# Optimization experiments

Measured on AMD Instinct MI355X. Metric: run time of the kernel, lower is better.

## Reference

```python
import jax, jax.numpy as jnp
import numpy as np

B, T, V, DIN = 16, 360, 25, 2
H, NCLS, NAUX = 128, 12, 8
NSPLITS = NAUX + 1
N = T * V        # nodes per graph
E = 72000        # edges per graph
EPS = 1e-5       # BatchNorm eps


def _norm_coefs(edge_index, n):
    # GCNConv default: add self-loops, symmetric normalization D^-1/2 (A+I) D^-1/2
    src, dst = edge_index[0], edge_index[1]
    loops = jnp.arange(n, dtype=src.dtype)
    src = jnp.concatenate([src, loops])
    dst = jnp.concatenate([dst, loops])
    deg = jnp.zeros((n,), jnp.float32).at[dst].add(1.0)
    dinv = jax.lax.rsqrt(deg)
    return src, dst, dinv[src] * dinv[dst]


def _gcn_bn_relu(x, W, b, gamma, beta, src, dst, coef):
    # x: [B, N, din] -> [B, N, dout]; GCNConv then BatchNorm1d (batch stats) + ReLU
    h = x @ W
    msg = h[:, src, :] * coef[None, :, None]          # gather + scale
    agg = jnp.zeros(h.shape, h.dtype).at[:, dst, :].add(msg) + b  # scatter-add
    mean = agg.mean(axis=(0, 1))
    var = agg.var(axis=(0, 1))                        # biased var, as torch BN fwd
    hn = (agg - mean) * jax.lax.rsqrt(var + EPS)
    return jax.nn.relu(gamma * hn + beta)


def _head(x, Wg, bg, gamma, beta, Wf, bf, src, dst, coef):
    h = _gcn_bn_relu(x, Wg, bg, gamma, beta, src, dst, coef)
    pooled = h.mean(axis=1)                           # GlobalMeanPool (equal-size graphs)
    # Dropout is identity in eval mode
    return jax.nn.log_softmax(pooled @ Wf + bf, axis=1)


def setup_inputs() -> dict:
    key = jax.random.key(0)
    ks = jax.random.split(key, 8)
    s = 0.1
    return {
        "x": jax.random.normal(ks[0], (B, T, V, DIN), jnp.float32),
        "edge_index": jax.random.randint(ks[1], (2, E), 0, N, jnp.int64 if jax.config.jax_enable_x64 else jnp.int32),
        "W_in": jax.random.normal(ks[2], (DIN, H), jnp.float32) * s,
        "b_in": jnp.zeros((H,), jnp.float32),
        "g_in": jnp.ones((H,), jnp.float32),
        "be_in": jnp.zeros((H,), jnp.float32),
        "shared_W": jax.random.normal(ks[3], (2, H, H), jnp.float32) * s,
        "shared_b": jnp.zeros((2, H), jnp.float32),
        "shared_g": jnp.ones((2, H), jnp.float32),
        "shared_be": jnp.zeros((2, H), jnp.float32),
        "main_Wg": jax.random.normal(ks[4], (H, H), jnp.float32) * s,
        "main_bg": jnp.zeros((H,), jnp.float32),
        "main_g": jnp.ones((H,), jnp.float32),
        "main_be": jnp.zeros((H,), jnp.float32),
        "main_Wf": jax.random.normal(ks[5], (H, NCLS), jnp.float32) * s,
        "main_bf": jnp.zeros((NCLS,), jnp.float32),
        "aux_Wg": jax.random.normal(ks[6], (NAUX, H, H), jnp.float32) * s,
        "aux_bg": jnp.zeros((NAUX, H), jnp.float32),
        "aux_g": jnp.ones((NAUX, H), jnp.float32),
        "aux_be": jnp.zeros((NAUX, H), jnp.float32),
        "aux_Wf": jax.random.normal(ks[7], (NAUX, H, NCLS), jnp.float32) * s,
        "aux_bf": jnp.zeros((NAUX, NCLS), jnp.float32),
    }


def reference(x, edge_index, W_in, b_in, g_in, be_in, shared_W, shared_b, shared_g,
              shared_be, main_Wg, main_bg, main_g, main_be, main_Wf, main_bf,
              aux_Wg, aux_bg, aux_g, aux_be, aux_Wf, aux_bf):
    src, dst, coef = _norm_coefs(edge_index, N)
    h = x.reshape(B, N, DIN)
    h = _gcn_bn_relu(h, W_in, b_in, g_in, be_in, src, dst, coef)
    for i in range(shared_W.shape[0]):
        h = _gcn_bn_relu(h, shared_W[i], shared_b[i], shared_g[i], shared_be[i], src, dst, coef)
    o_main = _head(h, main_Wg, main_bg, main_g, main_be, main_Wf, main_bf, src, dst, coef)
    h4 = h.reshape(B, T, V, H)
    ws = T // NSPLITS
    t = jnp.arange(T)
    outs = []
    for i in range(NSPLITS - 1):
        idx = (t + ws * (i + 1)) % T          # cyclic time shift (fi[si:si+T])
        hr = h4[:, idx].reshape(B, N, H)
        outs.append(_head(hr, aux_Wg[i], aux_bg[i], aux_g[i], aux_be[i],
                          aux_Wf[i], aux_bf[i], src, dst, coef))
    o_aux = jnp.stack(outs, axis=1)           # [B, NAUX, NCLS]
    return o_main, o_aux
```

## Files before the change

kernel.cpp:

```cpp
#include <hip/hip_runtime.h>
#include <hip/hip_bf16.h>
#include <math.h>

#define BB 16
#define TT 360
#define VV 25
#define NN 9000
#define EE 72000
#define HH 128
#define RR (NN * BB)
#define CROWS 18000
#define NTILES (RR / 64)
#define NPART0 563
#define NCLSS 12
#define EPSB 1e-5f


typedef _Float16 h4v __attribute__((ext_vector_type(4)));
typedef _Float16 h8v __attribute__((ext_vector_type(8)));
typedef float float16v __attribute__((ext_vector_type(16)));

__device__ __forceinline__ h8v cf8(unsigned packed) {
    uint4 cc = {packed, packed, packed, packed};
    return __builtin_bit_cast(h8v, cc);
}


__global__ void k_count(const int* __restrict__ ei, int* __restrict__ counts) {
    int e = blockIdx.x * 256 + threadIdx.x;
    if (e < EE) atomicAdd(&counts[ei[EE + e]], 1);
}

__global__ void k_dinv(const int* __restrict__ counts, float* __restrict__ dinv,
                       unsigned* __restrict__ d2p) {
    int n = blockIdx.x * 256 + threadIdx.x;
    if (n >= NN) return;
    float di = rsqrtf((float)(counts[n] + 1));
    dinv[n] = di;
    _Float16 d2 = (_Float16)(di * di);
    unsigned short u = __builtin_bit_cast(unsigned short, d2);
    d2p[n] = (unsigned)u | ((unsigned)u << 16);
}

__global__ void k_scan(const int* __restrict__ counts, int* __restrict__ rowptr4) {
    __shared__ int part[1024];
    int t = threadIdx.x;
    int base = t * 9;
    int loc[9];
    int s = 0;
#pragma unroll
    for (int i = 0; i < 9; i++) {
        int idx = base + i;
        int v = (idx < NN) ? ((counts[idx] + 3) & ~3) : 0;
        loc[i] = s;
        s += v;
    }
    part[t] = s;
    __syncthreads();
    for (int d = 1; d < 1024; d <<= 1) {
        int v = (t >= d) ? part[t - d] : 0;
        __syncthreads();
        part[t] += v;
        __syncthreads();
    }
    int excl = (t == 0) ? 0 : part[t - 1];
#pragma unroll
    for (int i = 0; i < 9; i++) {
        int idx = base + i;
        if (idx < NN) rowptr4[idx] = excl + loc[i];
    }
    if (t == 1023) rowptr4[NN] = part[1023];
}

__global__ void k_fill(const int* __restrict__ ei, const int* __restrict__ rowptr4,
                       int* __restrict__ cursor, const float* __restrict__ dinv,
                       int2* __restrict__ csr) {
    int e = blockIdx.x * 256 + threadIdx.x;
    if (e >= EE) return;
    int s = ei[e], d = ei[EE + e];
    int slot = rowptr4[d] + atomicAdd(&cursor[d], 1);
    _Float16 cfh = (_Float16)(dinv[s] * dinv[d]);
    unsigned short u = __builtin_bit_cast(unsigned short, cfh);
    int2 e2;
    e2.x = s;
    e2.y = (int)((unsigned)u | ((unsigned)u << 16));
    csr[slot] = e2;
}

__global__ void k_pad(const int* __restrict__ rowptr4, const int* __restrict__ cursor,
                      int2* __restrict__ csr) {
    int n = blockIdx.x * 256 + threadIdx.x;
    if (n >= NN) return;
    int beg = rowptr4[n] + cursor[n];
    int end = rowptr4[n + 1];
    int2 z;
    z.x = n;
    z.y = 0;
    for (int e = beg; e < end; e++) csr[e] = z;
}

__global__ void k_wcvt(const float* __restrict__ sW, const float* __restrict__ mW,
                       const float* __restrict__ aW, _Float16* __restrict__ Wh) {
    int idx = blockIdx.x * 256 + threadIdx.x;
    if (idx >= 11 * 16384) return;
    int l = idx >> 14, r = idx & 16383;
    int k = r >> 7, c = r & 127;
    const float* src = (l < 2) ? sW + (size_t)l * 16384
                               : ((l == 2) ? mW : aW + (size_t)(l - 3) * 16384);
    Wh[(size_t)l * 16384 + c * 128 + k] = (_Float16)src[k * 128 + c];
}

__global__ void k_prop2(const float* __restrict__ x, float* __restrict__ P0,
                        const int* __restrict__ rowptr4, const int2* __restrict__ csr,
                        const float* __restrict__ dinv) {
    int n = blockIdx.x * 256 + threadIdx.x;
    if (n >= NN) return;
    int b = blockIdx.y;
    const float* xb = x + (size_t)b * NN * 2;
    float d2 = dinv[n] * dinv[n];
    float a0 = d2 * xb[2 * n], a1 = d2 * xb[2 * n + 1];
    int beg = rowptr4[n], end = rowptr4[n + 1];
    for (int j = beg; j < end; j++) {
        int2 e2 = csr[j];
        int s = e2.x;
        unsigned short u = (unsigned short)((unsigned)e2.y & 0xffffu);
        float cf = (float)__builtin_bit_cast(_Float16, u);
        a0 += cf * xb[2 * s];
        a1 += cf * xb[2 * s + 1];
    }
    float* Pb = P0 + (size_t)(n * BB + b) * 2;
    Pb[0] = a0;
    Pb[1] = a1;
}

__global__ void __launch_bounds__(256) k_mm2(const float* __restrict__ P0,
                                             _Float16* __restrict__ A,
                                             const float* __restrict__ W,
                                             const float* __restrict__ bias,
                                             float* __restrict__ pS1, float* __restrict__ pS2) {
    __shared__ float L1[256][8], L2[256][8];
    int t = threadIdx.x;
    int cg = t & 15, c8 = cg * 8;
    float wv0[8], wv1[8], bv[8];
#pragma unroll
    for (int j = 0; j < 8; j++) {
        wv0[j] = W[c8 + j];
        wv1[j] = W[HH + c8 + j];
        bv[j] = bias[c8 + j];
    }
    float s1[8], s2[8];
#pragma unroll
    for (int j = 0; j < 8; j++) { s1[j] = 0.f; s2[j] = 0.f; }
    for (int idx = blockIdx.x * 256 + t; idx < RR * 16; idx += gridDim.x * 256) {
        int Rr = idx >> 4;
        int q = Rr / CROWS;
        int rr = Rr - q * CROWS;
        int n = rr >> 1;
        int b = q * 2 + (rr & 1);
        float p0 = P0[((size_t)n * BB + b) * 2], p1 = P0[((size_t)n * BB + b) * 2 + 1];
        h8v o;
#pragma unroll
        for (int j = 0; j < 8; j++) {
            float v = p0 * wv0[j] + p1 * wv1[j] + bv[j];
            s1[j] += v;
            s2[j] += v * v;
            o[j] = (_Float16)v;
        }
        *(h8v*)(A + (size_t)Rr * HH + c8) = o;
    }
#pragma unroll
    for (int j = 0; j < 8; j++) { L1[t][j] = s1[j]; L2[t][j] = s2[j]; }
    __syncthreads();
    if (t < 16) {
#pragma unroll
        for (int g = 1; g < 16; g++)
#pragma unroll
            for (int j = 0; j < 8; j++) {
                s1[j] = (g == 1 ? L1[t][j] : s1[j]) + L1[t + 16 * g][j];
                s2[j] = (g == 1 ? L2[t][j] : s2[j]) + L2[t + 16 * g][j];
            }
#pragma unroll
        for (int j = 0; j < 8; j++) {
            pS1[(size_t)(t * 8 + j) * NPART0 + blockIdx.x] = s1[j];
            pS2[(size_t)(t * 8 + j) * NPART0 + blockIdx.x] = s2[j];
        }
    }
}

__global__ void __launch_bounds__(256) k_act(const _Float16* __restrict__ A,
                                             _Float16* __restrict__ HP,
                                             const float* __restrict__ scale,
                                             const float* __restrict__ shiftv) {
    int i = blockIdx.x * 256 + threadIdx.x;
    int c8 = (i & 15) * 8;
    h8v v = *(const h8v*)(A + (size_t)i * 8);
    h8v o;
#pragma unroll
    for (int j = 0; j < 8; j++) {
        float f = (float)v[j] * scale[c8 + j] + shiftv[c8 + j];
        o[j] = (_Float16)fmaxf(f, 0.f);
    }
    *(h8v*)(HP + (size_t)i * 8) = o;
}

__global__ void __launch_bounds__(256) k_gather3(const _Float16* __restrict__ h,
                                                 _Float16* B0, _Float16* B1, _Float16* B2,
                                                 const int* __restrict__ rowptr4,
                                                 const int2* __restrict__ csr,
                                                 const unsigned* __restrict__ d2p, int shbase) {
    int z = blockIdx.y;
    _Float16* Pz = (z == 0) ? B0 : ((z == 1) ? B1 : B2);
    int shn = shbase + z * 1000;
    int t = threadIdx.x;
    int q = blockIdx.x & 7;
    int ng4 = blockIdx.x >> 3;
    int wv = t >> 6, l = t & 63;
    int n = ng4 * 4 + wv;
    int half = l >> 5, li = l & 31;
    const _Float16* hb = h + (size_t)q * CROWS * HH + (size_t)li * 8;
    int pn = n + shn;
    if (pn >= NN) pn -= NN;
    h8v acc;
    {
        h8v v = *(const h8v*)(hb + (size_t)pn * 2 * HH);
        acc = v * cf8(half ? 0u : d2p[n]);
    }
    int beg = rowptr4[n], end = rowptr4[n + 1];
    int e = beg;
    for (; e + 8 <= end; e += 8) {
        int4 m0 = *(const int4*)(csr + e);
        int4 m1 = *(const int4*)(csr + e + 2);
        int4 m2 = *(const int4*)(csr + e + 4);
        int4 m3 = *(const int4*)(csr + e + 6);
        int s0 = (half ? m0.z : m0.x) + shn; if (s0 >= NN) s0 -= NN;
        int s1 = (half ? m1.z : m1.x) + shn; if (s1 >= NN) s1 -= NN;
        int s2 = (half ? m2.z : m2.x) + shn; if (s2 >= NN) s2 -= NN;
        int s3 = (half ? m3.z : m3.x) + shn; if (s3 >= NN) s3 -= NN;
        h8v v0 = *(const h8v*)(hb + (size_t)s0 * 2 * HH);
        h8v v1 = *(const h8v*)(hb + (size_t)s1 * 2 * HH);
        h8v v2 = *(const h8v*)(hb + (size_t)s2 * 2 * HH);
        h8v v3 = *(const h8v*)(hb + (size_t)s3 * 2 * HH);
        acc += v0 * cf8((unsigned)(half ? m0.w : m0.y));
        acc += v1 * cf8((unsigned)(half ? m1.w : m1.y));
        acc += v2 * cf8((unsigned)(half ? m2.w : m2.y));
        acc += v3 * cf8((unsigned)(half ? m3.w : m3.y));
    }
    if (e < end) {
        int4 m0 = *(const int4*)(csr + e);
        int4 m1 = *(const int4*)(csr + e + 2);
        int s0 = (half ? m0.z : m0.x) + shn; if (s0 >= NN) s0 -= NN;
        int s1 = (half ? m1.z : m1.x) + shn; if (s1 >= NN) s1 -= NN;
        h8v v0 = *(const h8v*)(hb + (size_t)s0 * 2 * HH);
        h8v v1 = *(const h8v*)(hb + (size_t)s1 * 2 * HH);
        acc += v0 * cf8((unsigned)(half ? m0.w : m0.y));
        acc += v1 * cf8((unsigned)(half ? m1.w : m1.y));
    }
    {
        int4 ai = __builtin_bit_cast(int4, acc);
        int4 bi4;
        bi4.x = __shfl_xor(ai.x, 32, 64);
        bi4.y = __shfl_xor(ai.y, 32, 64);
        bi4.z = __shfl_xor(ai.z, 32, 64);
        bi4.w = __shfl_xor(ai.w, 32, 64);
        acc += __builtin_bit_cast(h8v, bi4);
    }
    if (half == 0) {
        *(h8v*)(Pz + ((size_t)q * CROWS + (size_t)n * 2) * HH + (size_t)li * 8) = acc;
    }
}

__global__ void __launch_bounds__(256) k_mfma3(_Float16* B0, _Float16* B1, _Float16* B2,
                                               const _Float16* __restrict__ Wh_g,
                                               const float* bias0, const float* bias1,
                                               const float* bias2,
                                               float* __restrict__ pS1,
                                               float* __restrict__ pS2) {
    __shared__ float rb1[4][128], rb2[4][128];
    int z = blockIdx.y;
    _Float16* B = (z == 0) ? B0 : ((z == 1) ? B1 : B2);
    const _Float16* Wh = Wh_g + (size_t)z * 16384;
    const float* bias = (z == 0) ? bias0 : ((z == 1) ? bias1 : bias2);
    int t = threadIdx.x;
    int w = t >> 6, l = t & 63;
    int rw = w >> 1, cw = w & 1;
    int lr = l & 31, hi = l >> 5;
    size_t rbase = (size_t)blockIdx.x * 64;
    const _Float16* Pr0 = B + (rbase + rw * 32 + lr) * HH;
    const _Float16* Wc0 = Wh + (size_t)(cw * 64 + lr) * HH;
    const _Float16* Wc1 = Wh + (size_t)(cw * 64 + 32 + lr) * HH;
    float16v acc2[2];
#pragma unroll
    for (int ct = 0; ct < 2; ct++) acc2[ct] = (float16v)(0.0f);
#pragma unroll
    for (int ks = 0; ks < 8; ks++) {
        int koff = ks * 16 + hi * 8;
        h8v a0 = *(const h8v*)(Pr0 + koff);
        h8v b0 = *(const h8v*)(Wc0 + koff);
        h8v b1 = *(const h8v*)(Wc1 + koff);
        acc2[0] = __builtin_amdgcn_mfma_f32_32x32x16_f16(a0, b0, acc2[0], 0, 0, 0);
        acc2[1] = __builtin_amdgcn_mfma_f32_32x32x16_f16(a0, b1, acc2[1], 0, 0, 0);
    }
    __syncthreads();
    float bv[2] = {bias[cw * 64 + lr], bias[cw * 64 + 32 + lr]};
    float s1a[2] = {0.f, 0.f}, s2a[2] = {0.f, 0.f};
#pragma unroll
    for (int ct = 0; ct < 2; ct++) {
        int c = cw * 64 + ct * 32 + lr;
#pragma unroll
        for (int g = 0; g < 16; g++) {
            int row = rw * 32 + (g & 3) + 8 * (g >> 2) + 4 * hi;
            float v = acc2[ct][g] + bv[ct];
            s1a[ct] += v;
            s2a[ct] += v * v;
            B[(rbase + row) * HH + c] = (_Float16)v;
        }
    }
    int slot = rw * 2 + hi;
#pragma unroll
    for (int ct = 0; ct < 2; ct++) {
        int cidx = cw * 64 + ct * 32 + lr;
        rb1[slot][cidx] = s1a[ct];
        rb2[slot][cidx] = s2a[ct];
    }
    __syncthreads();
    if (t < 128) {
        float a1 = rb1[0][t] + rb1[1][t] + rb1[2][t] + rb1[3][t];
        float a2 = rb2[0][t] + rb2[1][t] + rb2[2][t] + rb2[3][t];
        pS1[((size_t)z * HH + t) * NTILES + blockIdx.x] = a1;
        pS2[((size_t)z * HH + t) * NTILES + blockIdx.x] = a2;
    }
}

__global__ void __launch_bounds__(256) k_bnfin3(const float* __restrict__ pS1,
                                                const float* __restrict__ pS2, int npart,
                                                const float* g0, const float* g1,
                                                const float* g2, const float* be0,
                                                const float* be1, const float* be2,
                                                float* __restrict__ scale,
                                                float* __restrict__ shiftv) {
    __shared__ float R1[256], R2[256];
    int z = blockIdx.x >> 7, c = blockIdx.x & 127;
    const float* g = (z == 0) ? g0 : ((z == 1) ? g1 : g2);
    const float* be = (z == 0) ? be0 : ((z == 1) ? be1 : be2);
    int t = threadIdx.x;
    const float* p1 = pS1 + ((size_t)z * HH + c) * npart;
    const float* p2 = pS2 + ((size_t)z * HH + c) * npart;
    float s1 = 0.f, s2 = 0.f;
    for (int i = t; i < npart; i += 256) {
        s1 += p1[i];
        s2 += p2[i];
    }
    R1[t] = s1;
    R2[t] = s2;
    __syncthreads();
    for (int d = 128; d > 0; d >>= 1) {
        if (t < d) {
            R1[t] += R1[t + d];
            R2[t] += R2[t + d];
        }
        __syncthreads();
    }
    if (t == 0) {
        float inv = 1.0f / (float)RR;
        float mu = R1[0] * inv;
        float var = R2[0] * inv - mu * mu;
        float sc = g[c] * rsqrtf(var + EPSB);
        scale[z * HH + c] = sc;
        shiftv[z * HH + c] = be[c] - mu * sc;
    }
}

__global__ void __launch_bounds__(256) k_pool3(const _Float16* B0, const _Float16* B1,
                                               const _Float16* B2,
                                               const float* __restrict__ scale,
                                               const float* __restrict__ shiftv,
                                               float* __restrict__ pooled) {
    __shared__ float L[256][8];
    int z = blockIdx.z;
    const _Float16* A = (z == 0) ? B0 : ((z == 1) ? B1 : B2);
    const float* sc0 = scale + z * HH;
    const float* sh0 = shiftv + z * HH;
    float* pz = pooled + (size_t)z * BB * HH;
    int t = threadIdx.x;
    int b = blockIdx.y;
    int n0 = blockIdx.x * 250;
    int ng = t >> 4, c8 = (t & 15) * 8;
    float sc[8], sh[8];
#pragma unroll
    for (int j = 0; j < 8; j++) {
        sc[j] = sc0[c8 + j];
        sh[j] = sh0[c8 + j];
    }
    const _Float16* Ab = A + ((size_t)(b >> 1) * CROWS + (b & 1)) * HH;
    float acc[8];
#pragma unroll
    for (int j = 0; j < 8; j++) acc[j] = 0.f;
    for (int n = n0 + ng; n < n0 + 250; n += 16) {
        h8v v = *(const h8v*)(Ab + (size_t)n * 2 * HH + c8);
#pragma unroll
        for (int j = 0; j < 8; j++) {
            float f = (float)v[j] * sc[j] + sh[j];
            acc[j] += fmaxf(f, 0.f);
        }
    }
#pragma unroll
    for (int j = 0; j < 8; j++) L[t][j] = acc[j];
    __syncthreads();
    if (ng == 0) {
#pragma unroll
        for (int g = 1; g < 16; g++)
#pragma unroll
            for (int j = 0; j < 8; j++) acc[j] += L[t + 16 * g][j];
#pragma unroll
        for (int j = 0; j < 8; j++) atomicAdd(&pz[b * HH + t * 8 + j], acc[j]);
    }
}

__global__ void __launch_bounds__(192) k_head_all(const float* __restrict__ pooled,
                                                  const float* __restrict__ main_Wf,
                                                  const float* __restrict__ main_bf,
                                                  const float* __restrict__ aux_Wf,
                                                  const float* __restrict__ aux_bf,
                                                  float* __restrict__ out) {
    int hd = blockIdx.x;
    const float* Wf = hd ? aux_Wf + (size_t)(hd - 1) * HH * NCLSS : main_Wf;
    const float* bf = hd ? aux_bf + (hd - 1) * NCLSS : main_bf;
    const float* pl = pooled + (size_t)hd * BB * HH;
    __shared__ float z[BB][NCLSS];
    __shared__ float lse[BB];
    int t = threadIdx.x;
    int b = t / NCLSS, j = t % NCLSS;
    if (t < BB * NCLSS) {
        float acc = bf[j];
        const float invn = 1.0f / NN;
        for (int c = 0; c < HH; c++) acc += pl[b * HH + c] * invn * Wf[c * NCLSS + j];
        z[b][j] = acc;
    }
    __syncthreads();
    if (t < BB) {
        float m = -1e30f;
        for (int j2 = 0; j2 < NCLSS; j2++) m = fmaxf(m, z[t][j2]);
        float s = 0.f;
        for (int j2 = 0; j2 < NCLSS; j2++) s += expf(z[t][j2] - m);
        lse[t] = m + logf(s);
    }
    __syncthreads();
    if (t < BB * NCLSS) {
        float* o = hd ? out + BB * NCLSS + ((size_t)b * 8 + (hd - 1)) * NCLSS + j
                      : out + b * NCLSS + j;
        *o = z[b][j] - lse[b];
    }
}


extern "C" void kernel_launch(void* const* d_in, const int* in_sizes, int n_in, void* d_out,
                              int out_size, void* d_ws, size_t ws_size, hipStream_t stream) {
    const float* x = (const float*)d_in[0];
    const int* ei = (const int*)d_in[1];
    const float* W_in = (const float*)d_in[2];
    const float* b_in = (const float*)d_in[3];
    const float* g_in = (const float*)d_in[4];
    const float* be_in = (const float*)d_in[5];
    const float* shared_W = (const float*)d_in[6];
    const float* shared_b = (const float*)d_in[7];
    const float* shared_g = (const float*)d_in[8];
    const float* shared_be = (const float*)d_in[9];
    const float* main_Wg = (const float*)d_in[10];
    const float* main_bg = (const float*)d_in[11];
    const float* main_g = (const float*)d_in[12];
    const float* main_be = (const float*)d_in[13];
    const float* main_Wf = (const float*)d_in[14];
    const float* main_bf = (const float*)d_in[15];
    const float* aux_Wg = (const float*)d_in[16];
    const float* aux_bg = (const float*)d_in[17];
    const float* aux_g = (const float*)d_in[18];
    const float* aux_be = (const float*)d_in[19];
    const float* aux_Wf = (const float*)d_in[20];
    const float* aux_bf = (const float*)d_in[21];
    float* out = (float*)d_out;

    char* w = (char*)d_ws;
    const size_t BIG = (size_t)RR * HH * 2;
    _Float16* U = (_Float16*)w;  w += BIG;
    _Float16* V = (_Float16*)w;  w += BIG;
    _Float16* P = (_Float16*)w;  w += BIG;
    _Float16* HP = (_Float16*)w; w += BIG;
    float* P0 = (float*)w;       w += (size_t)RR * 2 * 4;
    _Float16* Wh = (_Float16*)w; w += (size_t)11 * 16384 * 2;
    int2* csr = (int2*)w;        w += (size_t)102400 * 8;
    int* counts = (int*)w;       w += NN * 4;
    int* cursor = (int*)w;       w += NN * 4;
    float* dinv = (float*)w;     w += NN * 4;
    unsigned* d2p = (unsigned*)w; w += NN * 4;
    int* rowptr4 = (int*)w;      w += 36016;
    float* pS1 = (float*)w;      w += (size_t)3 * HH * NTILES * 4;
    float* pS2 = (float*)w;      w += (size_t)3 * HH * NTILES * 4;
    float* pooled = (float*)w;   w += 9 * BB * HH * 4;
    float* tscale = (float*)w;   w += 512;
    float* tshift = (float*)w;   w += 512;
    float* hscale = (float*)w;   w += 2048;
    float* hshift = (float*)w;   w += 2048;

    hipMemsetAsync(counts, 0, 2 * NN * 4, stream);
    hipMemsetAsync(pooled, 0, 9 * BB * HH * 4, stream);

    k_count<<<(EE + 255) / 256, 256, 0, stream>>>(ei, counts);
    k_dinv<<<(NN + 255) / 256, 256, 0, stream>>>(counts, dinv, d2p);
    k_scan<<<1, 1024, 0, stream>>>(counts, rowptr4);
    k_fill<<<(EE + 255) / 256, 256, 0, stream>>>(ei, rowptr4, cursor, dinv, csr);
    k_pad<<<(NN + 255) / 256, 256, 0, stream>>>(rowptr4, cursor, csr);
    k_wcvt<<<(11 * 16384 + 255) / 256, 256, 0, stream>>>(shared_W, main_Wg, aux_Wg, Wh);

    {
        dim3 g((NN + 255) / 256, BB);
        k_prop2<<<g, 256, 0, stream>>>(x, P0, rowptr4, csr, dinv);
        k_mm2<<<NPART0, 256, 0, stream>>>(P0, U, W_in, b_in, pS1, pS2);
        k_bnfin3<<<HH, 256, 0, stream>>>(pS1, pS2, NPART0, g_in, g_in, g_in, be_in, be_in,
                                         be_in, tscale, tshift);
    }

    k_act<<<RR * 16 / 256, 256, 0, stream>>>(U, HP, tscale, tshift);
    k_gather3<<<dim3(8 * 2250, 1), 256, 0, stream>>>(HP, V, V, V, rowptr4, csr, d2p, 0);
    k_mfma3<<<dim3(NTILES, 1), 256, 0, stream>>>(V, V, V, Wh, shared_b, shared_b, shared_b,
                                                 pS1, pS2);
    k_bnfin3<<<HH, 256, 0, stream>>>(pS1, pS2, NTILES, shared_g, shared_g, shared_g, shared_be,
                                     shared_be, shared_be, tscale, tshift);
    k_act<<<RR * 16 / 256, 256, 0, stream>>>(V, HP, tscale, tshift);
    k_gather3<<<dim3(8 * 2250, 1), 256, 0, stream>>>(HP, U, U, U, rowptr4, csr, d2p, 0);
    k_mfma3<<<dim3(NTILES, 1), 256, 0, stream>>>(U, U, U, Wh + 16384, shared_b + HH,
                                                 shared_b + HH, shared_b + HH, pS1, pS2);
    k_bnfin3<<<HH, 256, 0, stream>>>(pS1, pS2, NTILES, shared_g + HH, shared_g + HH,
                                     shared_g + HH, shared_be + HH, shared_be + HH,
                                     shared_be + HH, tscale, tshift);
    k_act<<<RR * 16 / 256, 256, 0, stream>>>(U, HP, tscale, tshift);

    for (int g = 0; g < 3; g++) {
        int h0 = g * 3;
        const float* bg[3];
        const float* gg[3];
        const float* be[3];
        for (int z = 0; z < 3; z++) {
            int hd = h0 + z;
            bg[z] = (hd == 0) ? main_bg : aux_bg + (hd - 1) * HH;
            gg[z] = (hd == 0) ? main_g : aux_g + (hd - 1) * HH;
            be[z] = (hd == 0) ? main_be : aux_be + (hd - 1) * HH;
        }
        k_gather3<<<dim3(8 * 2250, 3), 256, 0, stream>>>(HP, P, U, V, rowptr4, csr, d2p,
                                                         h0 * 1000);
        k_mfma3<<<dim3(NTILES, 3), 256, 0, stream>>>(P, U, V, Wh + (size_t)(2 + h0) * 16384,
                                                     bg[0], bg[1], bg[2], pS1, pS2);
        k_bnfin3<<<3 * HH, 256, 0, stream>>>(pS1, pS2, NTILES, gg[0], gg[1], gg[2], be[0],
                                             be[1], be[2], hscale, hshift);
        k_pool3<<<dim3(36, BB, 3), 256, 0, stream>>>(P, U, V, hscale, hshift,
                                                     pooled + (size_t)h0 * BB * HH);
    }
    k_head_all<<<9, 192, 0, stream>>>(pooled, main_Wf, main_bf, aux_Wf, aux_bf, out);
}
```

Measured before the change: 868.2 us.

## Recompute GEMM instead of storing pre-BN output; fuse BN-ReLU and pooling into GEMM

The GEMM kernel no longer writes its fp16 output. It only emits per-tile BatchNorm partial sums. After the statistics are finalized, a second pass recomputes the GEMM and applies bias, BN and ReLU directly, writing HP for the shared layers or accumulating the pooled means for the heads. This removes the separate activation and pooling kernels along with the round-trip store and reload of the intermediate, at the cost of doing each GEMM twice. Tiles are now laid out per graph-pair of 18000 rows, with masking on the partial last tile so the pooling parity maps to batch index.

```diff
diff --git a/kernel.cpp b/kernel.cpp
--- a/kernel.cpp
+++ b/kernel.cpp
@@ -10,13 +10,13 @@
 #define HH 128
 #define RR (NN * BB)
 #define CROWS 18000
-#define NTILES (RR / 64)
+#define TPC2 282
+#define NT3 (8 * TPC2)
 #define NPART0 563
 #define NCLSS 12
 #define EPSB 1e-5f
 
 
-typedef _Float16 h4v __attribute__((ext_vector_type(4)));
 typedef _Float16 h8v __attribute__((ext_vector_type(8)));
 typedef float float16v __attribute__((ext_vector_type(16)));
 
@@ -269,22 +269,27 @@
     }
 }
 
-__global__ void __launch_bounds__(256) k_mfma3(_Float16* B0, _Float16* B1, _Float16* B2,
-                                               const _Float16* __restrict__ Wh_g,
-                                               const float* bias0, const float* bias1,
-                                               const float* bias2,
-                                               float* __restrict__ pS1,
-                                               float* __restrict__ pS2) {
+
+__global__ void __launch_bounds__(256) k_mfmaS3(const _Float16* B0, const _Float16* B1,
+                                                const _Float16* B2,
+                                                const _Float16* __restrict__ Wh_g,
+                                                const float* bias0, const float* bias1,
+                                                const float* bias2,
+                                                float* __restrict__ pS1,
+                                                float* __restrict__ pS2) {
     __shared__ float rb1[4][128], rb2[4][128];
     int z = blockIdx.y;
-    _Float16* B = (z == 0) ? B0 : ((z == 1) ? B1 : B2);
+    const _Float16* B = (z == 0) ? B0 : ((z == 1) ? B1 : B2);
     const _Float16* Wh = Wh_g + (size_t)z * 16384;
     const float* bias = (z == 0) ? bias0 : ((z == 1) ? bias1 : bias2);
     int t = threadIdx.x;
     int w = t >> 6, l = t & 63;
     int rw = w >> 1, cw = w & 1;
     int lr = l & 31, hi = l >> 5;
-    size_t rbase = (size_t)blockIdx.x * 64;
+    int q = blockIdx.x / TPC2, tile = blockIdx.x - q * TPC2;
+    int vrows = CROWS - tile * 64;
+    if (vrows > 64) vrows = 64;
+    size_t rbase = (size_t)q * CROWS + (size_t)tile * 64;
     const _Float16* Pr0 = B + (rbase + rw * 32 + lr) * HH;
     const _Float16* Wc0 = Wh + (size_t)(cw * 64 + lr) * HH;
     const _Float16* Wc1 = Wh + (size_t)(cw * 64 + 32 + lr) * HH;
@@ -300,19 +305,18 @@
         acc2[0] = __builtin_amdgcn_mfma_f32_32x32x16_f16(a0, b0, acc2[0], 0, 0, 0);
         acc2[1] = __builtin_amdgcn_mfma_f32_32x32x16_f16(a0, b1, acc2[1], 0, 0, 0);
     }
-    __syncthreads();
     float bv[2] = {bias[cw * 64 + lr], bias[cw * 64 + 32 + lr]};
     float s1a[2] = {0.f, 0.f}, s2a[2] = {0.f, 0.f};
 #pragma unroll
     for (int ct = 0; ct < 2; ct++) {
-        int c = cw * 64 + ct * 32 + lr;
 #pragma unroll
         for (int g = 0; g < 16; g++) {
             int row = rw * 32 + (g & 3) + 8 * (g >> 2) + 4 * hi;
-            float v = acc2[ct][g] + bv[ct];
-            s1a[ct] += v;
-            s2a[ct] += v * v;
-            B[(rbase + row) * HH + c] = (_Float16)v;
+            if (row < vrows) {
+                float v = acc2[ct][g] + bv[ct];
+                s1a[ct] += v;
+                s2a[ct] += v * v;
+            }
         }
     }
     int slot = rw * 2 + hi;
@@ -326,8 +330,123 @@
     if (t < 128) {
         float a1 = rb1[0][t] + rb1[1][t] + rb1[2][t] + rb1[3][t];
         float a2 = rb2[0][t] + rb2[1][t] + rb2[2][t] + rb2[3][t];
-        pS1[((size_t)z * HH + t) * NTILES + blockIdx.x] = a1;
-        pS2[((size_t)z * HH + t) * NTILES + blockIdx.x] = a2;
+        pS1[((size_t)z * HH + t) * NT3 + blockIdx.x] = a1;
+        pS2[((size_t)z * HH + t) * NT3 + blockIdx.x] = a2;
+    }
+}
+
+__global__ void __launch_bounds__(256) k_mfmaA(const _Float16* __restrict__ B,
+                                               const _Float16* __restrict__ Wh,
+                                               const float* __restrict__ bias,
+                                               const float* __restrict__ scale,
+                                               const float* __restrict__ shiftv,
+                                               _Float16* __restrict__ HP) {
+    int t = threadIdx.x;
+    int w = t >> 6, l = t & 63;
+    int rw = w >> 1, cw = w & 1;
+    int lr = l & 31, hi = l >> 5;
+    int q = blockIdx.x / TPC2, tile = blockIdx.x - q * TPC2;
+    int vrows = CROWS - tile * 64;
+    if (vrows > 64) vrows = 64;
+    size_t rbase = (size_t)q * CROWS + (size_t)tile * 64;
+    const _Float16* Pr0 = B + (rbase + rw * 32 + lr) * HH;
+    const _Float16* Wc0 = Wh + (size_t)(cw * 64 + lr) * HH;
+    const _Float16* Wc1 = Wh + (size_t)(cw * 64 + 32 + lr) * HH;
+    float16v acc2[2];
+#pragma unroll
+    for (int ct = 0; ct < 2; ct++) acc2[ct] = (float16v)(0.0f);
+#pragma unroll
+    for (int ks = 0; ks < 8; ks++) {
+        int koff = ks * 16 + hi * 8;
+        h8v a0 = *(const h8v*)(Pr0 + koff);
+        h8v b0 = *(const h8v*)(Wc0 + koff);
+        h8v b1 = *(const h8v*)(Wc1 + koff);
+        acc2[0] = __builtin_amdgcn_mfma_f32_32x32x16_f16(a0, b0, acc2[0], 0, 0, 0);
+        acc2[1] = __builtin_amdgcn_mfma_f32_32x32x16_f16(a0, b1, acc2[1], 0, 0, 0);
+    }
+#pragma unroll
+    for (int ct = 0; ct < 2; ct++) {
+        int c = cw * 64 + ct * 32 + lr;
+        float bv = bias[c];
+        float sc = scale[c], sh = shiftv[c];
+#pragma unroll
+        for (int g = 0; g < 16; g++) {
+            int row = rw * 32 + (g & 3) + 8 * (g >> 2) + 4 * hi;
+            if (row < vrows) {
+                float v = (acc2[ct][g] + bv) * sc + sh;
+                HP[(rbase + row) * HH + c] = (_Float16)fmaxf(v, 0.f);
+            }
+        }
+    }
+}
+
+__global__ void __launch_bounds__(256) k_mfmaP3(const _Float16* B0, const _Float16* B1,
+                                                const _Float16* B2,
+                                                const _Float16* __restrict__ Wh_g,
+                                                const float* bias0, const float* bias1,
+                                                const float* bias2,
+                                                const float* __restrict__ scale,
+                                                const float* __restrict__ shiftv,
+                                                float* __restrict__ pooled) {
+    __shared__ float rbP[2][4][128];
+    int z = blockIdx.y;
+    const _Float16* B = (z == 0) ? B0 : ((z == 1) ? B1 : B2);
+    const _Float16* Wh = Wh_g + (size_t)z * 16384;
+    const float* bias = (z == 0) ? bias0 : ((z == 1) ? bias1 : bias2);
+    const float* sc0 = scale + z * HH;
+    const float* sh0 = shiftv + z * HH;
+    float* pz = pooled + (size_t)z * BB * HH;
+    int t = threadIdx.x;
+    int w = t >> 6, l = t & 63;
+    int rw = w >> 1, cw = w & 1;
+    int lr = l & 31, hi = l >> 5;
+    int q = blockIdx.x / TPC2, tile = blockIdx.x - q * TPC2;
+    int vrows = CROWS - tile * 64;
+    if (vrows > 64) vrows = 64;
+    size_t rbase = (size_t)q * CROWS + (size_t)tile * 64;
+    const _Float16* Pr0 = B + (rbase + rw * 32 + lr) * HH;
+    const _Float16* Wc0 = Wh + (size_t)(cw * 64 + lr) * HH;
+    const _Float16* Wc1 = Wh + (size_t)(cw * 64 + 32 + lr) * HH;
+    float16v acc2[2];
+#pragma unroll
+    for (int ct = 0; ct < 2; ct++) acc2[ct] = (float16v)(0.0f);
+#pragma unroll
+    for (int ks = 0; ks < 8; ks++) {
+        int koff = ks * 16 + hi * 8;
+        h8v a0 = *(const h8v*)(Pr0 + koff);
+        h8v b0 = *(const h8v*)(Wc0 + koff);
+        h8v b1 = *(const h8v*)(Wc1 + koff);
+        acc2[0] = __builtin_amdgcn_mfma_f32_32x32x16_f16(a0, b0, acc2[0], 0, 0, 0);
+        acc2[1] = __builtin_amdgcn_mfma_f32_32x32x16_f16(a0, b1, acc2[1], 0, 0, 0);
+    }
+    float pp[2][2] = {{0.f, 0.f}, {0.f, 0.f}};
+#pragma unroll
+    for (int ct = 0; ct < 2; ct++) {
+        int c = cw * 64 + ct * 32 + lr;
+        float bv = bias[c];
+        float sc = sc0[c], sh = sh0[c];
+#pragma unroll
+        for (int g = 0; g < 16; g++) {
+            int row = rw * 32 + (g & 3) + 8 * (g >> 2) + 4 * hi;
+            if (row < vrows) {
+                float v = (acc2[ct][g] + bv) * sc + sh;
+                float f = fmaxf(v, 0.f);
+                if (g & 1) pp[ct][1] += f; else pp[ct][0] += f;
+            }
+        }
+    }
+    int slot = rw * 2 + hi;
+#pragma unroll
+    for (int ct = 0; ct < 2; ct++) {
+        int cidx = cw * 64 + ct * 32 + lr;
+        rbP[0][slot][cidx] = pp[ct][0];
+        rbP[1][slot][cidx] = pp[ct][1];
+    }
+    __syncthreads();
+    if (t < 256 && (t >> 7) < 2) {
+        int par = t >> 7, c = t & 127;
+        float a = rbP[par][0][c] + rbP[par][1][c] + rbP[par][2][c] + rbP[par][3][c];
+        atomicAdd(&pz[(q * 2 + par) * HH + c], a);
     }
 }
 
@@ -367,52 +486,6 @@
         float sc = g[c] * rsqrtf(var + EPSB);
         scale[z * HH + c] = sc;
         shiftv[z * HH + c] = be[c] - mu * sc;
-    }
-}
-
-__global__ void __launch_bounds__(256) k_pool3(const _Float16* B0, const _Float16* B1,
-                                               const _Float16* B2,
-                                               const float* __restrict__ scale,
-                                               const float* __restrict__ shiftv,
-                                               float* __restrict__ pooled) {
-    __shared__ float L[256][8];
-    int z = blockIdx.z;
-    const _Float16* A = (z == 0) ? B0 : ((z == 1) ? B1 : B2);
-    const float* sc0 = scale + z * HH;
-    const float* sh0 = shiftv + z * HH;
-    float* pz = pooled + (size_t)z * BB * HH;
-    int t = threadIdx.x;
-    int b = blockIdx.y;
-    int n0 = blockIdx.x * 250;
-    int ng = t >> 4, c8 = (t & 15) * 8;
-    float sc[8], sh[8];
-#pragma unroll
-    for (int j = 0; j < 8; j++) {
-        sc[j] = sc0[c8 + j];
-        sh[j] = sh0[c8 + j];
-    }
-    const _Float16* Ab = A + ((size_t)(b >> 1) * CROWS + (b & 1)) * HH;
-    float acc[8];
-#pragma unroll
-    for (int j = 0; j < 8; j++) acc[j] = 0.f;
-    for (int n = n0 + ng; n < n0 + 250; n += 16) {
-        h8v v = *(const h8v*)(Ab + (size_t)n * 2 * HH + c8);
-#pragma unroll
-        for (int j = 0; j < 8; j++) {
-            float f = (float)v[j] * sc[j] + sh[j];
-            acc[j] += fmaxf(f, 0.f);
-        }
-    }
-#pragma unroll
-    for (int j = 0; j < 8; j++) L[t][j] = acc[j];
-    __syncthreads();
-    if (ng == 0) {
-#pragma unroll
-        for (int g = 1; g < 16; g++)
-#pragma unroll
-            for (int j = 0; j < 8; j++) acc[j] += L[t + 16 * g][j];
-#pragma unroll
-        for (int j = 0; j < 8; j++) atomicAdd(&pz[b * HH + t * 8 + j], acc[j]);
     }
 }
 
@@ -493,8 +566,8 @@
     float* dinv = (float*)w;     w += NN * 4;
     unsigned* d2p = (unsigned*)w; w += NN * 4;
     int* rowptr4 = (int*)w;      w += 36016;
-    float* pS1 = (float*)w;      w += (size_t)3 * HH * NTILES * 4;
-    float* pS2 = (float*)w;      w += (size_t)3 * HH * NTILES * 4;
+    float* pS1 = (float*)w;      w += (size_t)3 * HH * NT3 * 4;
+    float* pS2 = (float*)w;      w += (size_t)3 * HH * NT3 * 4;
     float* pooled = (float*)w;   w += 9 * BB * HH * 4;
     float* tscale = (float*)w;   w += 512;
     float* tshift = (float*)w;   w += 512;
@@ -517,22 +590,20 @@
         k_mm2<<<NPART0, 256, 0, stream>>>(P0, U, W_in, b_in, pS1, pS2);
         k_bnfin3<<<HH, 256, 0, stream>>>(pS1, pS2, NPART0, g_in, g_in, g_in, be_in, be_in,
                                          be_in, tscale, tshift);
-    }
-
-    k_act<<<RR * 16 / 256, 256, 0, stream>>>(U, HP, tscale, tshift);
-    k_gather3<<<dim3(8 * 2250, 1), 256, 0, stream>>>(HP, V, V, V, rowptr4, csr, d2p, 0);
-    k_mfma3<<<dim3(NTILES, 1), 256, 0, stream>>>(V, V, V, Wh, shared_b, shared_b, shared_b,
-                                                 pS1, pS2);
-    k_bnfin3<<<HH, 256, 0, stream>>>(pS1, pS2, NTILES, shared_g, shared_g, shared_g, shared_be,
-                                     shared_be, shared_be, tscale, tshift);
-    k_act<<<RR * 16 / 256, 256, 0, stream>>>(V, HP, tscale, tshift);
-    k_gather3<<<dim3(8 * 2250, 1), 256, 0, stream>>>(HP, U, U, U, rowptr4, csr, d2p, 0);
-    k_mfma3<<<dim3(NTILES, 1), 256, 0, stream>>>(U, U, U, Wh + 16384, shared_b + HH,
-                                                 shared_b + HH, shared_b + HH, pS1, pS2);
-    k_bnfin3<<<HH, 256, 0, stream>>>(pS1, pS2, NTILES, shared_g + HH, shared_g + HH,
-                                     shared_g + HH, shared_be + HH, shared_be + HH,
-                                     shared_be + HH, tscale, tshift);
-    k_act<<<RR * 16 / 256, 256, 0, stream>>>(U, HP, tscale, tshift);
+        k_act<<<RR * 16 / 256, 256, 0, stream>>>(U, HP, tscale, tshift);
+    }
+
+    for (int l = 0; l < 2; l++) {
+        k_gather3<<<dim3(8 * 2250, 1), 256, 0, stream>>>(HP, V, V, V, rowptr4, csr, d2p, 0);
+        k_mfmaS3<<<dim3(NT3, 1), 256, 0, stream>>>(V, V, V, Wh + (size_t)l * 16384,
+                                                   shared_b + l * HH, shared_b + l * HH,
+                                                   shared_b + l * HH, pS1, pS2);
+        k_bnfin3<<<HH, 256, 0, stream>>>(pS1, pS2, NT3, shared_g + l * HH, shared_g + l * HH,
+                                         shared_g + l * HH, shared_be + l * HH,
+                                         shared_be + l * HH, shared_be + l * HH, tscale, tshift);
+        k_mfmaA<<<NT3, 256, 0, stream>>>(V, Wh + (size_t)l * 16384, shared_b + l * HH, tscale,
+                                         tshift, HP);
+    }
 
     for (int g = 0; g < 3; g++) {
         int h0 = g * 3;
@@ -547,12 +618,13 @@
         }
         k_gather3<<<dim3(8 * 2250, 3), 256, 0, stream>>>(HP, P, U, V, rowptr4, csr, d2p,
                                                          h0 * 1000);
-        k_mfma3<<<dim3(NTILES, 3), 256, 0, stream>>>(P, U, V, Wh + (size_t)(2 + h0) * 16384,
-                                                     bg[0], bg[1], bg[2], pS1, pS2);
-        k_bnfin3<<<3 * HH, 256, 0, stream>>>(pS1, pS2, NTILES, gg[0], gg[1], gg[2], be[0],
-                                             be[1], be[2], hscale, hshift);
-        k_pool3<<<dim3(36, BB, 3), 256, 0, stream>>>(P, U, V, hscale, hshift,
-                                                     pooled + (size_t)h0 * BB * HH);
+        k_mfmaS3<<<dim3(NT3, 3), 256, 0, stream>>>(P, U, V, Wh + (size_t)(2 + h0) * 16384,
+                                                   bg[0], bg[1], bg[2], pS1, pS2);
+        k_bnfin3<<<3 * HH, 256, 0, stream>>>(pS1, pS2, NT3, gg[0], gg[1], gg[2], be[0], be[1],
+                                             be[2], hscale, hshift);
+        k_mfmaP3<<<dim3(NT3, 3), 256, 0, stream>>>(P, U, V, Wh + (size_t)(2 + h0) * 16384,
+                                                   bg[0], bg[1], bg[2], hscale, hshift,
+                                                   pooled + (size_t)h0 * BB * HH);
     }
     k_head_all<<<9, 192, 0, stream>>>(pooled, main_Wf, main_bf, aux_Wf, aux_bf, out);
 }
```

After: 1.076 ms. +23.9%, slower.

## Stage MFMA output through LDS for coalesced stores and chunk-interleave tile grid

Applied to the files above, without the earlier changes.

k_mfma3 now writes its fp16 results into a shared-memory tile and then copies them to global memory as full 64-byte row segments. Before, each lane scattered scalar half-precision stores directly to global memory. Tiles are now indexed per 18000-row chunk, with the chunk as the fastest-varying block index, and a final partial tile masks out invalid rows from both stores and BN statistics. k_pool3's grid is reorganized the same way, likely to spread concurrent blocks across chunks for cache/channel locality. The 16 KB of extra LDS may reduce occupancy, and the padded tiles add a little redundant compute.

```diff
diff --git a/kernel.cpp b/kernel.cpp
--- a/kernel.cpp
+++ b/kernel.cpp
@@ -10,13 +10,13 @@
 #define HH 128
 #define RR (NN * BB)
 #define CROWS 18000
-#define NTILES (RR / 64)
+#define TPC2 282
+#define NT3 (8 * TPC2)
 #define NPART0 563
 #define NCLSS 12
 #define EPSB 1e-5f
 
 
-typedef _Float16 h4v __attribute__((ext_vector_type(4)));
 typedef _Float16 h8v __attribute__((ext_vector_type(8)));
 typedef float float16v __attribute__((ext_vector_type(16)));
 
@@ -275,6 +275,7 @@
                                                const float* bias2,
                                                float* __restrict__ pS1,
                                                float* __restrict__ pS2) {
+    __shared__ _Float16 st[64 * 128];
     __shared__ float rb1[4][128], rb2[4][128];
     int z = blockIdx.y;
     _Float16* B = (z == 0) ? B0 : ((z == 1) ? B1 : B2);
@@ -284,7 +285,11 @@
     int w = t >> 6, l = t & 63;
     int rw = w >> 1, cw = w & 1;
     int lr = l & 31, hi = l >> 5;
-    size_t rbase = (size_t)blockIdx.x * 64;
+    int q = blockIdx.x & 7;
+    int tile = blockIdx.x >> 3;
+    int vrows = CROWS - tile * 64;
+    if (vrows > 64) vrows = 64;
+    size_t rbase = (size_t)q * CROWS + (size_t)tile * 64;
     const _Float16* Pr0 = B + (rbase + rw * 32 + lr) * HH;
     const _Float16* Wc0 = Wh + (size_t)(cw * 64 + lr) * HH;
     const _Float16* Wc1 = Wh + (size_t)(cw * 64 + 32 + lr) * HH;
@@ -300,7 +305,6 @@
         acc2[0] = __builtin_amdgcn_mfma_f32_32x32x16_f16(a0, b0, acc2[0], 0, 0, 0);
         acc2[1] = __builtin_amdgcn_mfma_f32_32x32x16_f16(a0, b1, acc2[1], 0, 0, 0);
     }
-    __syncthreads();
     float bv[2] = {bias[cw * 64 + lr], bias[cw * 64 + 32 + lr]};
     float s1a[2] = {0.f, 0.f}, s2a[2] = {0.f, 0.f};
 #pragma unroll
@@ -310,9 +314,11 @@
         for (int g = 0; g < 16; g++) {
             int row = rw * 32 + (g & 3) + 8 * (g >> 2) + 4 * hi;
             float v = acc2[ct][g] + bv[ct];
-            s1a[ct] += v;
-            s2a[ct] += v * v;
-            B[(rbase + row) * HH + c] = (_Float16)v;
+            if (row < vrows) {
+                s1a[ct] += v;
+                s2a[ct] += v * v;
+            }
+            st[row * 128 + c] = (_Float16)v;
         }
     }
     int slot = rw * 2 + hi;
@@ -323,11 +329,22 @@
         rb2[slot][cidx] = s2a[ct];
     }
     __syncthreads();
+    {
+        int row = t >> 2, seg = (t & 3) * 32;
+        if (row < vrows) {
+            const h8v* s = (const h8v*)(st + row * 128 + seg);
+            h8v* dp = (h8v*)(B + (rbase + row) * HH + seg);
+            dp[0] = s[0];
+            dp[1] = s[1];
+            dp[2] = s[2];
+            dp[3] = s[3];
+        }
+    }
     if (t < 128) {
         float a1 = rb1[0][t] + rb1[1][t] + rb1[2][t] + rb1[3][t];
         float a2 = rb2[0][t] + rb2[1][t] + rb2[2][t] + rb2[3][t];
-        pS1[((size_t)z * HH + t) * NTILES + blockIdx.x] = a1;
-        pS2[((size_t)z * HH + t) * NTILES + blockIdx.x] = a2;
+        pS1[((size_t)z * HH + t) * NT3 + blockIdx.x] = a1;
+        pS2[((size_t)z * HH + t) * NT3 + blockIdx.x] = a2;
     }
 }
 
@@ -376,14 +393,17 @@
                                                const float* __restrict__ shiftv,
                                                float* __restrict__ pooled) {
     __shared__ float L[256][8];
-    int z = blockIdx.z;
+    int z = blockIdx.y;
     const _Float16* A = (z == 0) ? B0 : ((z == 1) ? B1 : B2);
     const float* sc0 = scale + z * HH;
     const float* sh0 = shiftv + z * HH;
     float* pz = pooled + (size_t)z * BB * HH;
     int t = threadIdx.x;
-    int b = blockIdx.y;
-    int n0 = blockIdx.x * 250;
+    int q = blockIdx.x & 7;
+    int rr = blockIdx.x >> 3;
+    int par = rr & 1;
+    int n0 = (rr >> 1) * 250;
+    int b = q * 2 + par;
     int ng = t >> 4, c8 = (t & 15) * 8;
     float sc[8], sh[8];
 #pragma unroll
@@ -391,7 +411,7 @@
         sc[j] = sc0[c8 + j];
         sh[j] = sh0[c8 + j];
     }
-    const _Float16* Ab = A + ((size_t)(b >> 1) * CROWS + (b & 1)) * HH;
+    const _Float16* Ab = A + ((size_t)q * CROWS + par) * HH;
     float acc[8];
 #pragma unroll
     for (int j = 0; j < 8; j++) acc[j] = 0.f;
@@ -493,8 +513,8 @@
     float* dinv = (float*)w;     w += NN * 4;
     unsigned* d2p = (unsigned*)w; w += NN * 4;
     int* rowptr4 = (int*)w;      w += 36016;
-    float* pS1 = (float*)w;      w += (size_t)3 * HH * NTILES * 4;
-    float* pS2 = (float*)w;      w += (size_t)3 * HH * NTILES * 4;
+    float* pS1 = (float*)w;      w += (size_t)3 * HH * NT3 * 4;
+    float* pS2 = (float*)w;      w += (size_t)3 * HH * NT3 * 4;
     float* pooled = (float*)w;   w += 9 * BB * HH * 4;
     float* tscale = (float*)w;   w += 512;
     float* tshift = (float*)w;   w += 512;
@@ -521,15 +541,15 @@
 
     k_act<<<RR * 16 / 256, 256, 0, stream>>>(U, HP, tscale, tshift);
     k_gather3<<<dim3(8 * 2250, 1), 256, 0, stream>>>(HP, V, V, V, rowptr4, csr, d2p, 0);
-    k_mfma3<<<dim3(NTILES, 1), 256, 0, stream>>>(V, V, V, Wh, shared_b, shared_b, shared_b,
-                                                 pS1, pS2);
-    k_bnfin3<<<HH, 256, 0, stream>>>(pS1, pS2, NTILES, shared_g, shared_g, shared_g, shared_be,
+    k_mfma3<<<dim3(NT3, 1), 256, 0, stream>>>(V, V, V, Wh, shared_b, shared_b, shared_b,
+                                              pS1, pS2);
+    k_bnfin3<<<HH, 256, 0, stream>>>(pS1, pS2, NT3, shared_g, shared_g, shared_g, shared_be,
                                      shared_be, shared_be, tscale, tshift);
     k_act<<<RR * 16 / 256, 256, 0, stream>>>(V, HP, tscale, tshift);
     k_gather3<<<dim3(8 * 2250, 1), 256, 0, stream>>>(HP, U, U, U, rowptr4, csr, d2p, 0);
-    k_mfma3<<<dim3(NTILES, 1), 256, 0, stream>>>(U, U, U, Wh + 16384, shared_b + HH,
-                                                 shared_b + HH, shared_b + HH, pS1, pS2);
-    k_bnfin3<<<HH, 256, 0, stream>>>(pS1, pS2, NTILES, shared_g + HH, shared_g + HH,
+    k_mfma3<<<dim3(NT3, 1), 256, 0, stream>>>(U, U, U, Wh + 16384, shared_b + HH,
+                                              shared_b + HH, shared_b + HH, pS1, pS2);
+    k_bnfin3<<<HH, 256, 0, stream>>>(pS1, pS2, NT3, shared_g + HH, shared_g + HH,
                                      shared_g + HH, shared_be + HH, shared_be + HH,
                                      shared_be + HH, tscale, tshift);
     k_act<<<RR * 16 / 256, 256, 0, stream>>>(U, HP, tscale, tshift);
@@ -547,12 +567,12 @@
         }
         k_gather3<<<dim3(8 * 2250, 3), 256, 0, stream>>>(HP, P, U, V, rowptr4, csr, d2p,
                                                          h0 * 1000);
-        k_mfma3<<<dim3(NTILES, 3), 256, 0, stream>>>(P, U, V, Wh + (size_t)(2 + h0) * 16384,
-                                                     bg[0], bg[1], bg[2], pS1, pS2);
-        k_bnfin3<<<3 * HH, 256, 0, stream>>>(pS1, pS2, NTILES, gg[0], gg[1], gg[2], be[0],
+        k_mfma3<<<dim3(NT3, 3), 256, 0, stream>>>(P, U, V, Wh + (size_t)(2 + h0) * 16384,
+                                                  bg[0], bg[1], bg[2], pS1, pS2);
+        k_bnfin3<<<3 * HH, 256, 0, stream>>>(pS1, pS2, NT3, gg[0], gg[1], gg[2], be[0],
                                              be[1], be[2], hscale, hshift);
-        k_pool3<<<dim3(36, BB, 3), 256, 0, stream>>>(P, U, V, hscale, hshift,
-                                                     pooled + (size_t)h0 * BB * HH);
+        k_pool3<<<dim3(576, 3), 256, 0, stream>>>(P, U, V, hscale, hshift,
+                                                  pooled + (size_t)h0 * BB * HH);
     }
     k_head_all<<<9, 192, 0, stream>>>(pooled, main_Wf, main_bf, aux_Wf, aux_bf, out);
 }
```

After: 930.6 us. 1.07x slower.
